# Kernel optimization log

Measured on AMD Instinct MI355X. Metric: run time of the kernel, lower is better.

The kernel has to match this reference:

```python
import jax, jax.numpy as jnp
import numpy as np
import math


def _omega_np(nrows: int, ncols: int, rng: np.random.RandomState) -> np.ndarray:
    # Block-orthogonal random feature matrix, transposed to (ncols, nrows)
    nblocks = int(nrows / ncols)
    blocks = []
    for _ in range(nblocks):
        q, _ = np.linalg.qr(rng.normal(size=(ncols, ncols)))
        blocks.append(q.T)
    missing = nrows - nblocks * ncols
    if missing > 0:
        q, _ = np.linalg.qr(rng.normal(size=(ncols, ncols)))
        blocks.append(q.T[:missing])
    norm = np.linalg.norm(rng.normal(size=(nrows, ncols)), axis=1, keepdims=True)
    return (norm * np.vstack(blocks)).T  # (ncols, nrows) = (dim_qk, m)


def setup_inputs() -> dict:
    N, DIM_QK, DIM_V, M = 262144, 128, 128, 256
    key = jax.random.key(0)
    kq, kk, kv = jax.random.split(key, 3)
    Q = jax.random.normal(kq, (N, DIM_QK), dtype=jnp.float32)
    K = jax.random.normal(kk, (N, DIM_QK), dtype=jnp.float32)
    V = jax.random.normal(kv, (N, DIM_V), dtype=jnp.float32)
    omega = jnp.asarray(_omega_np(M, DIM_QK, np.random.RandomState(0)), dtype=jnp.float32)
    return {"Q": Q, "K": K, "V": V, "omega": omega}


def _phi(X, omega, is_query: bool, eps: float = 1e-4):
    d = X.shape[-1]
    m = omega.shape[-1]
    U = jnp.matmul(X / d ** 0.25, omega)                       # [N, m]
    h = jnp.sum(X * X, axis=-1, keepdims=True) / (2.0 * d ** 0.5)
    if is_query:
        maximum = jnp.max(U, axis=-1, keepdims=True)
    else:
        maximum = jnp.max(U)
    return (jnp.exp(U - h - maximum) + eps) / math.sqrt(m)


def reference(Q, K, V, omega):
    eps = 1e-8
    Qp = _phi(Q, omega, True)    # [N, m]
    Kp = _phi(K, omega, False)   # [N, m]
    norm = Qp @ jnp.sum(Kp, axis=0) + eps                       # [N]
    # Faithful to einsum('nF,nF,nf->nf', Qp, Kp, V): row-wise dot * V
    w = jnp.sum(Qp * Kp, axis=-1, keepdims=True)                # [N, 1]
    return w * V / norm[:, None]                                # [N, dim_v]
```

## Files before the change

kernel.cpp:

```cpp
#include <hip/hip_runtime.h>
#include <hip/hip_bf16.h>


typedef _Float16 f16x8 __attribute__((ext_vector_type(8)));
typedef float f32x4 __attribute__((ext_vector_type(4)));

#define D_QK 128
#define M_F  256
#define OMS  136

constexpr float D4      = 0.29730177875068026f;
constexpr float H_SCALE = 0.044194173824159216f;

__device__ __forceinline__ unsigned f2key(float f) {
  unsigned b = __float_as_uint(f);
  return (b & 0x80000000u) ? ~b : (b | 0x80000000u);
}
__device__ __forceinline__ float key2f(unsigned k) {
  return (k & 0x80000000u) ? __uint_as_float(k & 0x7fffffffu) : __uint_as_float(~k);
}

__device__ __forceinline__ f32x4 mfma16(f16x8 a, f16x8 b, f32x4 c) {
  return __builtin_amdgcn_mfma_f32_16x16x32_f16(a, b, c, 0, 0, 0);
}

__device__ __forceinline__ void load_frag(const float* __restrict__ row, int ks, int q,
                                          f16x8& a, float& h) {
  const float4* p = (const float4*)(row + ks * 32 + q * 8);
  float4 x0 = p[0], x1 = p[1];
  h += x0.x*x0.x + x0.y*x0.y + x0.z*x0.z + x0.w*x0.w
     + x1.x*x1.x + x1.y*x1.y + x1.z*x1.z + x1.w*x1.w;
  a[0] = (_Float16)(x0.x * D4); a[1] = (_Float16)(x0.y * D4);
  a[2] = (_Float16)(x0.z * D4); a[3] = (_Float16)(x0.w * D4);
  a[4] = (_Float16)(x1.x * D4); a[5] = (_Float16)(x1.y * D4);
  a[6] = (_Float16)(x1.z * D4); a[7] = (_Float16)(x1.w * D4);
}

extern "C" __global__ void k_prep(const float* __restrict__ om, _Float16* __restrict__ omt,
                                  float* __restrict__ S, unsigned* __restrict__ Mkey) {
  int i = blockIdx.x * 256 + threadIdx.x;
  if (i < D_QK * M_F) {
    int m = i >> 7, d = i & 127;
    omt[m * OMS + d] = (_Float16)om[d * M_F + m];
  }
  if (blockIdx.x == 0) {
    S[threadIdx.x] = 0.f;
    if (threadIdx.x == 0) *Mkey = 0u;
  }
}

__global__ __launch_bounds__(256, 4) void k_kstats(
    const float* __restrict__ K, const _Float16* __restrict__ omt,
    float* __restrict__ Lout, float* __restrict__ Pout, unsigned* __restrict__ Mkey) {
  __shared__ _Float16 om_lds[128 * OMS];
  __shared__ float P_lds[4][256];
  __shared__ float red_lds[4];
  int tid = threadIdx.x;
  int w = tid >> 6, lane = tid & 63, q = lane >> 4, c = lane & 15;
  int rb = blockIdx.x * 64 + w * 16;

  const float* krow = K + (size_t)(rb + c) * D_QK;
  f16x8 ak[4];
  float hk = 0.f;
#pragma unroll
  for (int ks = 0; ks < 4; ++ks) load_frag(krow, ks, q, ak[ks], hk);
  hk += __shfl_xor(hk, 16, 64);
  hk += __shfl_xor(hk, 32, 64);
  hk *= H_SCALE;

  const f32x4 zero = {0.f, 0.f, 0.f, 0.f};
  f32x4 cc[16];
#pragma unroll
  for (int t = 0; t < 16; ++t) cc[t] = zero;

  const float4* osrc = (const float4*)omt;
  float4* odst = (float4*)om_lds;
  for (int i = tid; i < 2176; i += 256) odst[i] = osrc[i];
  __syncthreads();
#pragma unroll
  for (int t = 0; t < 8; ++t) {
#pragma unroll
    for (int ks = 0; ks < 4; ++ks) {
      f16x8 b = *(const f16x8*)&om_lds[(t * 16 + c) * OMS + ks * 32 + q * 8];
      cc[t] = mfma16(ak[ks], b, cc[t]);
    }
  }
  __syncthreads();
  for (int i = tid; i < 2176; i += 256) odst[i] = osrc[i + 2176];
  __syncthreads();
#pragma unroll
  for (int t = 8; t < 16; ++t) {
#pragma unroll
    for (int ks = 0; ks < 4; ++ks) {
      f16x8 b = *(const f16x8*)&om_lds[((t - 8) * 16 + c) * OMS + ks * 32 + q * 8];
      cc[t] = mfma16(ak[ks], b, cc[t]);
    }
  }

  float mx = cc[0][0];
#pragma unroll
  for (int t = 0; t < 16; ++t)
    mx = fmaxf(mx, fmaxf(fmaxf(cc[t][0], cc[t][1]), fmaxf(cc[t][2], cc[t][3])));
#pragma unroll
  for (int m = 1; m <= 32; m <<= 1) mx = fmaxf(mx, __shfl_xor(mx, m, 64));
  if (lane == 0) red_lds[w] = mx;
  __syncthreads();
  float Lb = fmaxf(fmaxf(red_lds[0], red_lds[1]), fmaxf(red_lds[2], red_lds[3]));

  float hr[4];
#pragma unroll
  for (int r = 0; r < 4; ++r) hr[r] = __shfl(hk, q * 4 + r, 64);

#pragma unroll
  for (int t = 0; t < 16; ++t) {
    float s = __expf(cc[t][0] - hr[0] - Lb) + __expf(cc[t][1] - hr[1] - Lb)
            + __expf(cc[t][2] - hr[2] - Lb) + __expf(cc[t][3] - hr[3] - Lb);
    s += __shfl_xor(s, 16, 64);
    s += __shfl_xor(s, 32, 64);
    if (q == 0) P_lds[w][t * 16 + c] = s;
  }
  __syncthreads();
  Pout[(size_t)blockIdx.x * 256 + tid] =
      P_lds[0][tid] + P_lds[1][tid] + P_lds[2][tid] + P_lds[3][tid];
  if (tid == 0) {
    Lout[blockIdx.x] = Lb;
    atomicMax(Mkey, f2key(Lb));
  }
}

extern "C" __global__ void k_combine(const float* __restrict__ Lout, const float* __restrict__ Pout,
                                     const unsigned* __restrict__ Mkey, float* __restrict__ Mout,
                                     float* __restrict__ S) {
  float M = key2f(*Mkey);
  if (blockIdx.x == 0 && threadIdx.x == 0) *Mout = M;
  int b0 = blockIdx.x * 32;
  float acc = 0.f;
  for (int i = 0; i < 32; ++i) {
    int b = b0 + i;
    float f = __expf(Lout[b] - M);
    acc += f * Pout[(size_t)b * 256 + threadIdx.x];
  }
  atomicAdd(&S[threadIdx.x], acc);
}

__global__ __launch_bounds__(256, 2) void k_main(
    const float* __restrict__ Q, const float* __restrict__ K, const float* __restrict__ V,
    const _Float16* __restrict__ omt, const float* __restrict__ Sws,
    const float* __restrict__ Mws, float* __restrict__ out, float epsN) {
  __shared__ _Float16 om_lds[128 * OMS];
  __shared__ float S_lds[256];
  __shared__ float scale_lds[64];
  int tid = threadIdx.x;
  int w = tid >> 6, lane = tid & 63, q = lane >> 4, c = lane & 15;
  int rb = blockIdx.x * 64 + w * 16;

  S_lds[tid] = (Sws[tid] + epsN) * 0.0625f;
  float Mglob = *Mws;

  const float* qrow = Q + (size_t)(rb + c) * D_QK;
  const float* krow = K + (size_t)(rb + c) * D_QK;
  f16x8 aq[4], ak[4];
  float hq = 0.f, hk = 0.f;
#pragma unroll
  for (int ks = 0; ks < 4; ++ks) {
    load_frag(qrow, ks, q, aq[ks], hq);
    load_frag(krow, ks, q, ak[ks], hk);
  }
  hq += __shfl_xor(hq, 16, 64); hq += __shfl_xor(hq, 32, 64); hq *= H_SCALE;
  hk += __shfl_xor(hk, 16, 64); hk += __shfl_xor(hk, 32, 64); hk *= H_SCALE;

  const f32x4 zero = {0.f, 0.f, 0.f, 0.f};
  f32x4 cq[16], ck[16];
#pragma unroll
  for (int t = 0; t < 16; ++t) { cq[t] = zero; ck[t] = zero; }

  const float4* osrc = (const float4*)omt;
  float4* odst = (float4*)om_lds;
  for (int i = tid; i < 2176; i += 256) odst[i] = osrc[i];
  __syncthreads();
#pragma unroll
  for (int t = 0; t < 8; ++t) {
#pragma unroll
    for (int ks = 0; ks < 4; ++ks) {
      f16x8 b = *(const f16x8*)&om_lds[(t * 16 + c) * OMS + ks * 32 + q * 8];
      cq[t] = mfma16(aq[ks], b, cq[t]);
      ck[t] = mfma16(ak[ks], b, ck[t]);
    }
  }
  __syncthreads();
  for (int i = tid; i < 2176; i += 256) odst[i] = osrc[i + 2176];
  __syncthreads();
#pragma unroll
  for (int t = 8; t < 16; ++t) {
#pragma unroll
    for (int ks = 0; ks < 4; ++ks) {
      f16x8 b = *(const f16x8*)&om_lds[((t - 8) * 16 + c) * OMS + ks * 32 + q * 8];
      cq[t] = mfma16(aq[ks], b, cq[t]);
      ck[t] = mfma16(ak[ks], b, ck[t]);
    }
  }

  float hqr[4], hkr[4];
#pragma unroll
  for (int r = 0; r < 4; ++r) {
    hqr[r] = __shfl(hq, q * 4 + r, 64);
    hkr[r] = __shfl(hk, q * 4 + r, 64);
  }

#pragma unroll
  for (int r = 0; r < 4; ++r) {
    float mx = cq[0][r];
#pragma unroll
    for (int t = 1; t < 16; ++t) mx = fmaxf(mx, cq[t][r]);
#pragma unroll
    for (int m = 1; m <= 8; m <<= 1) mx = fmaxf(mx, __shfl_xor(mx, m, 64));
    float wsum = 0.f, nsum = 0.f;
#pragma unroll
    for (int t = 0; t < 16; ++t) {
      float qp = __expf(cq[t][r] - hqr[r] - mx) + 1e-4f;
      float kp = __expf(ck[t][r] - hkr[r] - Mglob) + 1e-4f;
      wsum += qp * kp;
      nsum += qp * S_lds[t * 16 + c];
    }
#pragma unroll
    for (int m = 1; m <= 8; m <<= 1) {
      wsum += __shfl_xor(wsum, m, 64);
      nsum += __shfl_xor(nsum, m, 64);
    }
    if (c == 0)
      scale_lds[w * 16 + q * 4 + r] = (wsum * (1.f / 256.f)) / (nsum * 0.0625f + 1e-8f);
  }
  __syncthreads();

  const float4* vsrc = (const float4*)(V + (size_t)blockIdx.x * 64 * D_QK);
  float4* odst4 = (float4*)(out + (size_t)blockIdx.x * 64 * D_QK);
#pragma unroll
  for (int i = 0; i < 8; ++i) {
    int j = tid + i * 256;
    float s = scale_lds[j >> 5];
    float4 v = vsrc[j];
    odst4[j] = make_float4(v.x * s, v.y * s, v.z * s, v.w * s);
  }
}

extern "C" void kernel_launch(void* const* d_in, const int* in_sizes, int n_in,
                              void* d_out, int out_size, void* d_ws, size_t ws_size,
                              hipStream_t stream) {
  const float* Q  = (const float*)d_in[0];
  const float* K  = (const float*)d_in[1];
  const float* V  = (const float*)d_in[2];
  const float* om = (const float*)d_in[3];
  float* out = (float*)d_out;
  int N = in_sizes[0] / D_QK;
  int nblk = N / 64;

  char* ws = (char*)d_ws;
  _Float16* omt = (_Float16*)ws;
  size_t off = (size_t)M_F * OMS * 2;
  float* Lout = (float*)(ws + off);   off += (size_t)nblk * 4;
  float* Pout = (float*)(ws + off);   off += (size_t)nblk * 256 * 4;
  float* S    = (float*)(ws + off);   off += 1024;
  unsigned* Mkey = (unsigned*)(ws + off); off += 16;
  float* Mout = (float*)(ws + off);

  hipLaunchKernelGGL(k_prep, dim3((D_QK * M_F + 255) / 256), dim3(256), 0, stream,
                     om, omt, S, Mkey);
  hipLaunchKernelGGL(k_kstats, dim3(nblk), dim3(256), 0, stream, K, omt, Lout, Pout, Mkey);
  hipLaunchKernelGGL(k_combine, dim3(nblk / 32), dim3(256), 0, stream, Lout, Pout, Mkey, Mout, S);
  hipLaunchKernelGGL(k_main, dim3(nblk), dim3(256), 0, stream, Q, K, V, omt, S, Mout, out,
                     (float)N * 1e-4f);
}
```

Before: 516.7 us.

## Pre-swizzle omega into MFMA fragment order and stage the full matrix in LDS once

Omega is now stored in global memory already arranged in per-lane MFMA B-fragment order. Each block loads the whole 64KB matrix into registers, writes it to LDS with a single barrier, and reads conflict-free contiguous fragments. This replaces the two-phase half-matrix staging with its extra syncs, and the global loads are issued before the row loads so their latency overlaps. The combine kernel now uses more blocks with fewer iterations each. The costs are higher LDS use per block (kstats occupancy hint drops from 4 to 2), 16 extra float4 registers, and more atomics in combine.

New measurement: 450.2 us. -12.9%, faster.

```diff
diff --git a/kernel.cpp b/kernel.cpp
--- a/kernel.cpp
+++ b/kernel.cpp
@@ -7,7 +7,7 @@
 
 #define D_QK 128
 #define M_F  256
-#define OMS  136
+#define OMT_HALVES 32768
 
 constexpr float D4      = 0.29730177875068026f;
 constexpr float H_SCALE = 0.044194173824159216f;
@@ -36,12 +36,18 @@
   a[6] = (_Float16)(x1.z * D4); a[7] = (_Float16)(x1.w * D4);
 }
 
+__device__ __forceinline__ f16x8 bfrag(const _Float16* om_lds, int t, int ks, int lane) {
+  return *(const f16x8*)&om_lds[(((t << 2) | ks) << 9) + (lane << 3)];
+}
+
 extern "C" __global__ void k_prep(const float* __restrict__ om, _Float16* __restrict__ omt,
                                   float* __restrict__ S, unsigned* __restrict__ Mkey) {
   int i = blockIdx.x * 256 + threadIdx.x;
-  if (i < D_QK * M_F) {
-    int m = i >> 7, d = i & 127;
-    omt[m * OMS + d] = (_Float16)om[d * M_F + m];
+  if (i < OMT_HALVES) {
+    int t = i >> 11, ks = (i >> 9) & 3, l = (i >> 3) & 63, j = i & 7;
+    int d = ks * 32 + ((l >> 4) << 3) + j;
+    int m = t * 16 + (l & 15);
+    omt[i] = (_Float16)om[d * M_F + m];
   }
   if (blockIdx.x == 0) {
     S[threadIdx.x] = 0.f;
@@ -49,16 +55,21 @@
   }
 }
 
-__global__ __launch_bounds__(256, 4) void k_kstats(
+__global__ __launch_bounds__(256, 2) void k_kstats(
     const float* __restrict__ K, const _Float16* __restrict__ omt,
     float* __restrict__ Lout, float* __restrict__ Pout, unsigned* __restrict__ Mkey) {
-  __shared__ _Float16 om_lds[128 * OMS];
+  __shared__ __align__(16) _Float16 om_lds[OMT_HALVES];
   __shared__ float P_lds[4][256];
   __shared__ float red_lds[4];
   int tid = threadIdx.x;
   int w = tid >> 6, lane = tid & 63, q = lane >> 4, c = lane & 15;
   int rb = blockIdx.x * 64 + w * 16;
 
+  const float4* osrc = (const float4*)omt;
+  float4 st[16];
+#pragma unroll
+  for (int i = 0; i < 16; ++i) st[i] = osrc[tid + i * 256];
+
   const float* krow = K + (size_t)(rb + c) * D_QK;
   f16x8 ak[4];
   float hk = 0.f;
@@ -68,31 +79,21 @@
   hk += __shfl_xor(hk, 32, 64);
   hk *= H_SCALE;
 
+  float4* odst = (float4*)om_lds;
+#pragma unroll
+  for (int i = 0; i < 16; ++i) odst[tid + i * 256] = st[i];
+
   const f32x4 zero = {0.f, 0.f, 0.f, 0.f};
   f32x4 cc[16];
 #pragma unroll
   for (int t = 0; t < 16; ++t) cc[t] = zero;
-
-  const float4* osrc = (const float4*)omt;
-  float4* odst = (float4*)om_lds;
-  for (int i = tid; i < 2176; i += 256) odst[i] = osrc[i];
-  __syncthreads();
-#pragma unroll
-  for (int t = 0; t < 8; ++t) {
+  __syncthreads();
+
+#pragma unroll
+  for (int t = 0; t < 16; ++t) {
 #pragma unroll
     for (int ks = 0; ks < 4; ++ks) {
-      f16x8 b = *(const f16x8*)&om_lds[(t * 16 + c) * OMS + ks * 32 + q * 8];
-      cc[t] = mfma16(ak[ks], b, cc[t]);
-    }
-  }
-  __syncthreads();
-  for (int i = tid; i < 2176; i += 256) odst[i] = osrc[i + 2176];
-  __syncthreads();
-#pragma unroll
-  for (int t = 8; t < 16; ++t) {
-#pragma unroll
-    for (int ks = 0; ks < 4; ++ks) {
-      f16x8 b = *(const f16x8*)&om_lds[((t - 8) * 16 + c) * OMS + ks * 32 + q * 8];
+      f16x8 b = bfrag(om_lds, t, ks, lane);
       cc[t] = mfma16(ak[ks], b, cc[t]);
     }
   }
@@ -133,9 +134,10 @@
                                      float* __restrict__ S) {
   float M = key2f(*Mkey);
   if (blockIdx.x == 0 && threadIdx.x == 0) *Mout = M;
-  int b0 = blockIdx.x * 32;
+  int b0 = blockIdx.x * 8;
   float acc = 0.f;
-  for (int i = 0; i < 32; ++i) {
+#pragma unroll
+  for (int i = 0; i < 8; ++i) {
     int b = b0 + i;
     float f = __expf(Lout[b] - M);
     acc += f * Pout[(size_t)b * 256 + threadIdx.x];
@@ -147,13 +149,18 @@
     const float* __restrict__ Q, const float* __restrict__ K, const float* __restrict__ V,
     const _Float16* __restrict__ omt, const float* __restrict__ Sws,
     const float* __restrict__ Mws, float* __restrict__ out, float epsN) {
-  __shared__ _Float16 om_lds[128 * OMS];
+  __shared__ __align__(16) _Float16 om_lds[OMT_HALVES];
   __shared__ float S_lds[256];
   __shared__ float scale_lds[64];
   int tid = threadIdx.x;
   int w = tid >> 6, lane = tid & 63, q = lane >> 4, c = lane & 15;
   int rb = blockIdx.x * 64 + w * 16;
 
+  const float4* osrc = (const float4*)omt;
+  float4 st[16];
+#pragma unroll
+  for (int i = 0; i < 16; ++i) st[i] = osrc[tid + i * 256];
+
   S_lds[tid] = (Sws[tid] + epsN) * 0.0625f;
   float Mglob = *Mws;
 
@@ -169,32 +176,21 @@
   hq += __shfl_xor(hq, 16, 64); hq += __shfl_xor(hq, 32, 64); hq *= H_SCALE;
   hk += __shfl_xor(hk, 16, 64); hk += __shfl_xor(hk, 32, 64); hk *= H_SCALE;
 
+  float4* odst = (float4*)om_lds;
+#pragma unroll
+  for (int i = 0; i < 16; ++i) odst[tid + i * 256] = st[i];
+
   const f32x4 zero = {0.f, 0.f, 0.f, 0.f};
   f32x4 cq[16], ck[16];
 #pragma unroll
   for (int t = 0; t < 16; ++t) { cq[t] = zero; ck[t] = zero; }
-
-  const float4* osrc = (const float4*)omt;
-  float4* odst = (float4*)om_lds;
-  for (int i = tid; i < 2176; i += 256) odst[i] = osrc[i];
-  __syncthreads();
-#pragma unroll
-  for (int t = 0; t < 8; ++t) {
+  __syncthreads();
+
+#pragma unroll
+  for (int t = 0; t < 16; ++t) {
 #pragma unroll
     for (int ks = 0; ks < 4; ++ks) {
-      f16x8 b = *(const f16x8*)&om_lds[(t * 16 + c) * OMS + ks * 32 + q * 8];
-      cq[t] = mfma16(aq[ks], b, cq[t]);
-      ck[t] = mfma16(ak[ks], b, ck[t]);
-    }
-  }
-  __syncthreads();
-  for (int i = tid; i < 2176; i += 256) odst[i] = osrc[i + 2176];
-  __syncthreads();
-#pragma unroll
-  for (int t = 8; t < 16; ++t) {
-#pragma unroll
-    for (int ks = 0; ks < 4; ++ks) {
-      f16x8 b = *(const f16x8*)&om_lds[((t - 8) * 16 + c) * OMS + ks * 32 + q * 8];
+      f16x8 b = bfrag(om_lds, t, ks, lane);
       cq[t] = mfma16(aq[ks], b, cq[t]);
       ck[t] = mfma16(ak[ks], b, ck[t]);
     }
@@ -256,17 +252,17 @@
 
   char* ws = (char*)d_ws;
   _Float16* omt = (_Float16*)ws;
-  size_t off = (size_t)M_F * OMS * 2;
+  size_t off = (size_t)OMT_HALVES * 2;
   float* Lout = (float*)(ws + off);   off += (size_t)nblk * 4;
   float* Pout = (float*)(ws + off);   off += (size_t)nblk * 256 * 4;
   float* S    = (float*)(ws + off);   off += 1024;
   unsigned* Mkey = (unsigned*)(ws + off); off += 16;
   float* Mout = (float*)(ws + off);
 
-  hipLaunchKernelGGL(k_prep, dim3((D_QK * M_F + 255) / 256), dim3(256), 0, stream,
+  hipLaunchKernelGGL(k_prep, dim3((OMT_HALVES + 255) / 256), dim3(256), 0, stream,
                      om, omt, S, Mkey);
   hipLaunchKernelGGL(k_kstats, dim3(nblk), dim3(256), 0, stream, K, omt, Lout, Pout, Mkey);
-  hipLaunchKernelGGL(k_combine, dim3(nblk / 32), dim3(256), 0, stream, Lout, Pout, Mkey, Mout, S);
+  hipLaunchKernelGGL(k_combine, dim3(nblk / 8), dim3(256), 0, stream, Lout, Pout, Mkey, Mout, S);
   hipLaunchKernelGGL(k_main, dim3(nblk), dim3(256), 0, stream, Q, K, V, omt, S, Mout, out,
                      (float)N * 1e-4f);
 }
```
